# Kernel optimization log

Measured on AMD Instinct MI355X. Metric: run time of the kernel, lower is better.

## Reference

```python
import jax, jax.numpy as jnp
import numpy as np

DIM_IN, DIM_H, DIM_OUT = 1024, 512, 256
E, T, B = 8, 4, 16384


def setup_inputs() -> dict:
    key = jax.random.key(0)
    ks = jax.random.split(key, 8)
    s1 = 1.0 / np.sqrt(DIM_IN)
    s2 = 1.0 / np.sqrt(DIM_H)
    x = jax.random.normal(ks[0], (B, DIM_IN), dtype=jnp.float32)
    # stacked expert params: layer1 [E, H, IN], layer2 [E, OUT, H]
    W1 = jax.random.uniform(ks[1], (E, DIM_H, DIM_IN), jnp.float32, -s1, s1)
    b1 = jax.random.uniform(ks[2], (E, DIM_H), jnp.float32, -s1, s1)
    W2 = jax.random.uniform(ks[3], (E, DIM_OUT, DIM_H), jnp.float32, -s2, s2)
    b2 = jax.random.uniform(ks[4], (E, DIM_OUT), jnp.float32, -s2, s2)
    # gate params: [T, E, IN]
    Wg = jax.random.uniform(ks[5], (T, E, DIM_IN), jnp.float32, -s1, s1)
    bg = jax.random.uniform(ks[6], (T, E), jnp.float32, -s1, s1)
    return {"x": x, "W1": W1, "b1": b1, "W2": W2, "b2": b2, "Wg": Wg, "bg": bg}


def reference(x, W1, b1, W2, b2, Wg, bg):
    # Experts: Linear+ReLU, Linear+ReLU (dropout=0 / eval mode)
    h = jax.nn.relu(jnp.einsum('bi,ehi->beh', x, W1) + b1)          # [B,E,H]
    feats = jax.nn.relu(jnp.einsum('beh,edh->bed', h, W2) + b2)     # [B,E,D]
    # Gates: softmax over experts, one gate per task
    logits = jnp.einsum('bi,tei->bte', x, Wg) + bg                  # [B,T,E]
    w = jax.nn.softmax(logits, axis=-1)                             # [B,T,E]
    # Weighted combine: einsum('bde,be->bd') per task
    out = jnp.einsum('bed,bte->tbd', feats, w)                      # [T,B,D]
    return out
```

## Files before the change

### kernel.cpp

```cpp
#include <hip/hip_runtime.h>


typedef __attribute__((ext_vector_type(8))) __bf16 bf16x8;
typedef __attribute__((ext_vector_type(4))) float f32x4;
typedef __attribute__((ext_vector_type(8))) unsigned short u16x8;

__device__ __forceinline__ float bf2f(unsigned short u) {
  union { unsigned int i; float f; } x;
  x.i = ((unsigned int)u) << 16;
  return x.f;
}

__device__ __forceinline__ unsigned short f2bf(float f) {
  union { float f; unsigned int i; } x;
  x.f = f;
  unsigned int r = x.i + 0x7FFFu + ((x.i >> 16) & 1u);
  return (unsigned short)(r >> 16);
}

__device__ __forceinline__ void gload_lds16(const unsigned short* g, unsigned short* l) {
  __builtin_amdgcn_global_load_lds(
      (const __attribute__((address_space(1))) void*)g,
      (__attribute__((address_space(3))) void*)l, 16, 0, 0);
}

__global__ void cvt_k(const float* __restrict__ in, unsigned short* __restrict__ out, int n4) {
  int i = blockIdx.x * blockDim.x + threadIdx.x;
  if (i >= n4) return;
  float4 v = ((const float4*)in)[i];
  ushort4 o;
  o.x = f2bf(v.x); o.y = f2bf(v.y); o.z = f2bf(v.z); o.w = f2bf(v.w);
  ((ushort4*)out)[i] = o;
}

__global__ __launch_bounds__(256) void gates_k(
    const unsigned short* __restrict__ xb,
    const unsigned short* __restrict__ Wgb,
    const float* __restrict__ bg,
    float* __restrict__ gw)
{
  const int lane = threadIdx.x & 63;
  const int wid = threadIdx.x >> 6;
  const int wgid = blockIdx.x * 4 + wid;
  const int brow = wgid * 16;
  const int l15 = lane & 15, lhi = lane >> 4;

  f32x4 acc0 = {0.f, 0.f, 0.f, 0.f};
  f32x4 acc1 = {0.f, 0.f, 0.f, 0.f};
  for (int k0 = 0; k0 < 1024; k0 += 32) {
    bf16x8 a  = *(const bf16x8*)&xb[(size_t)(brow + l15) * 1024 + k0 + lhi * 8];
    bf16x8 b0 = *(const bf16x8*)&Wgb[(size_t)l15 * 1024 + k0 + lhi * 8];
    bf16x8 b1 = *(const bf16x8*)&Wgb[(size_t)(16 + l15) * 1024 + k0 + lhi * 8];
    acc0 = __builtin_amdgcn_mfma_f32_16x16x32_bf16(a, b0, acc0, 0, 0, 0);
    acc1 = __builtin_amdgcn_mfma_f32_16x16x32_bf16(a, b1, acc1, 0, 0, 0);
  }
  const float bg0 = bg[l15];
  const float bg1 = bg[16 + l15];
#pragma unroll
  for (int r = 0; r < 4; ++r) {
    float v0 = acc0[r] + bg0;
    float v1 = acc1[r] + bg1;
    float m0 = v0, m1 = v1;
#pragma unroll
    for (int d = 1; d <= 4; d <<= 1) {
      m0 = fmaxf(m0, __shfl_xor(m0, d));
      m1 = fmaxf(m1, __shfl_xor(m1, d));
    }
    float e0 = __expf(v0 - m0), e1 = __expf(v1 - m1);
    float s0 = e0, s1 = e1;
#pragma unroll
    for (int d = 1; d <= 4; d <<= 1) {
      s0 += __shfl_xor(s0, d);
      s1 += __shfl_xor(s1, d);
    }
    int b = brow + lhi * 4 + r;
    gw[(size_t)b * 32 + l15]      = e0 / s0;
    gw[(size_t)b * 32 + 16 + l15] = e1 / s1;
  }
}

template <bool RELU>
__global__ __launch_bounds__(512, 2) void gemm256(
    const unsigned short* __restrict__ A, int lda, int aZ,
    const unsigned short* __restrict__ B,
    const float* __restrict__ bias,
    unsigned short* __restrict__ C, int ldc, int cZ,
    int tilesN, int N, int K)
{
  extern __shared__ char smem_raw[];
  unsigned short* lds = (unsigned short*)smem_raw;
  char* ldsb = (char*)smem_raw;

  const int tid = threadIdx.x;
  const int lane = tid & 63, wid = tid >> 6;
  const int wr = wid >> 2, wc = wid & 3;
  const int l15 = lane & 15, lhi = lane >> 4;

  const int nwg = gridDim.x;
  const int cpx = nwg >> 3;
  const int wg = blockIdx.x;
  const int swz = (wg & 7) * cpx + (wg >> 3);
  const int rt = swz / tilesN, ct = swz - rt * tilesN;
  const int brow = rt * 256, bcol = ct * 256;
  const int e = blockIdx.z;

  const unsigned short* Ab = A + (size_t)e * aZ + (size_t)brow * lda;
  const unsigned short* Bb = B + (size_t)e * N * K + (size_t)bcol * K;
  const float* biasb = bias + (size_t)e * N;
  unsigned short* Cb = C + (size_t)e * cZ;

  const int NT = K >> 6;
  const int NI = NT >> 1;

  const int trow = tid >> 3;
  const int cg8 = (((tid & 7) ^ (trow & 7)) << 3);

  const int axor = (l15 & 7) << 4;
  const int koff0 = (lhi << 4) ^ axor;
  const int koff1 = (64 + (lhi << 4)) ^ axor;

  const char* pA0 = ldsb + wr * 16384 + l15 * 128 + koff0;
  const char* pA1 = ldsb + wr * 16384 + l15 * 128 + koff1;
  const char* pB0 = ldsb + 65536 + wc * 8192 + l15 * 128 + koff0;
  const char* pB1 = ldsb + 65536 + wc * 8192 + l15 * 128 + koff1;

  const f32x4 zero = {0.f, 0.f, 0.f, 0.f};
  f32x4 acc[8][4];
#pragma unroll
  for (int m = 0; m < 8; ++m)
#pragma unroll
    for (int n = 0; n < 4; ++n) acc[m][n] = zero;

  auto STAGE_A = [&](int slot, int t, int u) {
    gload_lds16(Ab + (size_t)(u * 64 + trow) * lda + (t * 64 + cg8),
                lds + slot * 16384 + u * 4096 + wid * 512);
  };
  auto STAGE_B = [&](int slot, int t, int u) {
    gload_lds16(Bb + (size_t)(u * 64 + trow) * K + (t * 64 + cg8),
                lds + 32768 + slot * 16384 + u * 4096 + wid * 512);
  };

#pragma unroll
  for (int u = 0; u < 4; ++u) STAGE_B(0, 0, u);
  STAGE_A(0, 0, 0); STAGE_A(0, 0, 2);
  STAGE_A(0, 0, 1); STAGE_A(0, 0, 3);
#pragma unroll
  for (int u = 0; u < 4; ++u) STAGE_B(1, 1, u);
  asm volatile("s_waitcnt vmcnt(6)" ::: "memory");
  __builtin_amdgcn_s_barrier();

  auto ktile = [&](int slot, int t) {
    const bool stA = (t + 1) < NT;
    const bool stB = (t + 2) < NT;
    bf16x8 af[4][2], bfr[4][2];

#pragma unroll
    for (int mi = 0; mi < 4; ++mi) {
      af[mi][0] = *(const bf16x8*)(pA0 + slot * 32768 + mi * 2048);
      af[mi][1] = *(const bf16x8*)(pA1 + slot * 32768 + mi * 2048);
    }
#pragma unroll
    for (int n = 0; n < 2; ++n) {
      bfr[n][0] = *(const bf16x8*)(pB0 + slot * 32768 + n * 2048);
      bfr[n][1] = *(const bf16x8*)(pB1 + slot * 32768 + n * 2048);
    }
    if (stA) { STAGE_A(slot ^ 1, t + 1, 0); STAGE_A(slot ^ 1, t + 1, 2); }
    __builtin_amdgcn_s_barrier();
    __builtin_amdgcn_s_setprio(1);
#pragma unroll
    for (int kk = 0; kk < 2; ++kk)
#pragma unroll
      for (int mi = 0; mi < 4; ++mi)
#pragma unroll
        for (int n = 0; n < 2; ++n)
          acc[mi][n] = __builtin_amdgcn_mfma_f32_16x16x32_bf16(bfr[n][kk], af[mi][kk], acc[mi][n], 0, 0, 0);
    __builtin_amdgcn_s_setprio(0);
    __builtin_amdgcn_s_barrier();

#pragma unroll
    for (int n = 0; n < 2; ++n) {
      bfr[2 + n][0] = *(const bf16x8*)(pB0 + slot * 32768 + (2 + n) * 2048);
      bfr[2 + n][1] = *(const bf16x8*)(pB1 + slot * 32768 + (2 + n) * 2048);
    }
    if (stA) { STAGE_A(slot ^ 1, t + 1, 1); STAGE_A(slot ^ 1, t + 1, 3); }
    __builtin_amdgcn_s_barrier();
    __builtin_amdgcn_s_setprio(1);
#pragma unroll
    for (int kk = 0; kk < 2; ++kk)
#pragma unroll
      for (int mi = 0; mi < 4; ++mi)
#pragma unroll
        for (int n = 0; n < 2; ++n)
          acc[mi][2 + n] = __builtin_amdgcn_mfma_f32_16x16x32_bf16(bfr[2 + n][kk], af[mi][kk], acc[mi][2 + n], 0, 0, 0);
    __builtin_amdgcn_s_setprio(0);
    if (stA) asm volatile("s_waitcnt vmcnt(8)" ::: "memory");
    else     asm volatile("s_waitcnt vmcnt(0)" ::: "memory");
    __builtin_amdgcn_s_barrier();

#pragma unroll
    for (int mi = 0; mi < 4; ++mi) {
      af[mi][0] = *(const bf16x8*)(pA0 + slot * 32768 + 8192 + mi * 2048);
      af[mi][1] = *(const bf16x8*)(pA1 + slot * 32768 + 8192 + mi * 2048);
    }
    if (stB) { STAGE_B(slot, t + 2, 0); STAGE_B(slot, t + 2, 1); }
    __builtin_amdgcn_s_barrier();
    __builtin_amdgcn_s_setprio(1);
#pragma unroll
    for (int kk = 0; kk < 2; ++kk)
#pragma unroll
      for (int mi = 0; mi < 4; ++mi)
#pragma unroll
        for (int n = 0; n < 2; ++n)
          acc[4 + mi][n] = __builtin_amdgcn_mfma_f32_16x16x32_bf16(bfr[n][kk], af[mi][kk], acc[4 + mi][n], 0, 0, 0);
    __builtin_amdgcn_s_setprio(0);
    __builtin_amdgcn_s_barrier();

    if (stB) { STAGE_B(slot, t + 2, 2); STAGE_B(slot, t + 2, 3); }
    __builtin_amdgcn_s_barrier();
    __builtin_amdgcn_s_setprio(1);
#pragma unroll
    for (int kk = 0; kk < 2; ++kk)
#pragma unroll
      for (int mi = 0; mi < 4; ++mi)
#pragma unroll
        for (int n = 0; n < 2; ++n)
          acc[4 + mi][2 + n] = __builtin_amdgcn_mfma_f32_16x16x32_bf16(bfr[2 + n][kk], af[mi][kk], acc[4 + mi][2 + n], 0, 0, 0);
    __builtin_amdgcn_s_setprio(0);
    if (stB) {
      asm volatile("s_waitcnt vmcnt(6)" ::: "memory");
      __builtin_amdgcn_s_barrier();
    } else if (stA) {
      asm volatile("s_waitcnt vmcnt(2)" ::: "memory");
      __builtin_amdgcn_s_barrier();
    }
  };

#pragma unroll 1
  for (int i = 0; i < NI; ++i) {
    ktile(0, 2 * i);
    ktile(1, 2 * i + 1);
  }

  f32x4 bias4[4];
#pragma unroll
  for (int nf = 0; nf < 4; ++nf)
    bias4[nf] = *(const f32x4*)&biasb[bcol + wc * 64 + nf * 16 + lhi * 4];

#pragma unroll
  for (int mf = 0; mf < 8; ++mf) {
    const size_t rowoff = (size_t)(brow + wr * 128 + mf * 16 + l15) * ldc;
#pragma unroll
    for (int nf = 0; nf < 4; ++nf) {
      const int col = bcol + wc * 64 + nf * 16 + lhi * 4;
      f32x4 v = acc[mf][nf];
      ushort4 o;
      float v0 = v[0] + bias4[nf][0];
      float v1 = v[1] + bias4[nf][1];
      float v2 = v[2] + bias4[nf][2];
      float v3 = v[3] + bias4[nf][3];
      if (RELU) {
        v0 = v0 > 0.f ? v0 : 0.f;
        v1 = v1 > 0.f ? v1 : 0.f;
        v2 = v2 > 0.f ? v2 : 0.f;
        v3 = v3 > 0.f ? v3 : 0.f;
      }
      o.x = f2bf(v0); o.y = f2bf(v1); o.z = f2bf(v2); o.w = f2bf(v3);
      *(ushort4*)&Cb[rowoff + col] = o;
    }
  }
}

template <bool RELU>
__global__ __launch_bounds__(256) void gemm_bt(
    const unsigned short* __restrict__ A, int lda, int aZ,
    const unsigned short* __restrict__ B,
    const float* __restrict__ bias,
    unsigned short* __restrict__ C, int ldc, int cZ,
    int N, int K)
{
  __shared__ unsigned short As[128 * 64];
  __shared__ unsigned short Bs[128 * 64];
  const int tid = threadIdx.x;
  const int wid = tid >> 6;
  const int lane = tid & 63;
  const int wr = wid >> 1, wc = wid & 1;
  const int l15 = lane & 15, lhi = lane >> 4;
  const int brow = blockIdx.x * 128;
  const int bcol = blockIdx.y * 128;
  const int e = blockIdx.z;

  const unsigned short* Ab = A + (size_t)e * aZ;
  const unsigned short* Bb = B + (size_t)e * N * K;
  const float* biasb = bias + (size_t)e * N;
  unsigned short* Cb = C + (size_t)e * cZ;

  const f32x4 zero = {0.f, 0.f, 0.f, 0.f};
  f32x4 acc[4][4];
#pragma unroll
  for (int m = 0; m < 4; ++m)
#pragma unroll
    for (int n = 0; n < 4; ++n) acc[m][n] = zero;

  const int srow = lane >> 3;
  const int scol = (lane & 7) * 8;
  const int rbase = wid * 32;

  for (int k0 = 0; k0 < K; k0 += 64) {
#pragma unroll
    for (int i = 0; i < 4; ++i) {
      int r = rbase + i * 8;
      gload_lds16(Ab + (size_t)(brow + r + srow) * lda + (k0 + scol), &As[r * 64]);
    }
#pragma unroll
    for (int i = 0; i < 4; ++i) {
      int r = rbase + i * 8;
      gload_lds16(Bb + (size_t)(bcol + r + srow) * K + (k0 + scol), &Bs[r * 64]);
    }
    __syncthreads();
#pragma unroll
    for (int kk = 0; kk < 2; ++kk) {
      bf16x8 af[4], bfr[4];
#pragma unroll
      for (int m = 0; m < 4; ++m)
        af[m] = *(const bf16x8*)&As[(wr * 64 + m * 16 + l15) * 64 + kk * 32 + lhi * 8];
#pragma unroll
      for (int n = 0; n < 4; ++n)
        bfr[n] = *(const bf16x8*)&Bs[(wc * 64 + n * 16 + l15) * 64 + kk * 32 + lhi * 8];
#pragma unroll
      for (int m = 0; m < 4; ++m)
#pragma unroll
        for (int n = 0; n < 4; ++n)
          acc[m][n] = __builtin_amdgcn_mfma_f32_16x16x32_bf16(af[m], bfr[n], acc[m][n], 0, 0, 0);
    }
    __syncthreads();
  }

#pragma unroll
  for (int n = 0; n < 4; ++n) {
    int col = bcol + wc * 64 + n * 16 + l15;
    float bv = biasb[col];
#pragma unroll
    for (int m = 0; m < 4; ++m) {
      int row0 = brow + wr * 64 + m * 16 + lhi * 4;
#pragma unroll
      for (int r = 0; r < 4; ++r) {
        float v = acc[m][n][r] + bv;
        if (RELU) v = v > 0.f ? v : 0.f;
        Cb[(size_t)(row0 + r) * ldc + col] = f2bf(v);
      }
    }
  }
}

__global__ __launch_bounds__(256) void combine_k(
    const unsigned short* __restrict__ feats,
    const float* __restrict__ gw,
    float* __restrict__ out)
{
  int tid = blockIdx.x * 256 + threadIdx.x;
  int b = tid >> 5;
  int d0 = (tid & 31) * 8;

  const f32x4* wv4 = (const f32x4*)(gw + (size_t)b * 32);
  f32x4 wv[8];
#pragma unroll
  for (int i = 0; i < 8; ++i) wv[i] = wv4[i];

  float o[4][8];
#pragma unroll
  for (int t = 0; t < 4; ++t)
#pragma unroll
    for (int j = 0; j < 8; ++j) o[t][j] = 0.f;

#pragma unroll
  for (int e = 0; e < 8; ++e) {
    u16x8 fv = *(const u16x8*)&feats[((size_t)b * 8 + e) * 256 + d0];
    float f[8];
#pragma unroll
    for (int j = 0; j < 8; ++j) f[j] = bf2f(fv[j]);
#pragma unroll
    for (int t = 0; t < 4; ++t) {
      float wt = wv[(t * 8 + e) >> 2][(t * 8 + e) & 3];
#pragma unroll
      for (int j = 0; j < 8; ++j) o[t][j] += wt * f[j];
    }
  }
#pragma unroll
  for (int t = 0; t < 4; ++t) {
    f32x4* dst = (f32x4*)(out + ((size_t)t * 16384 + b) * 256 + d0);
    f32x4 s0 = {o[t][0], o[t][1], o[t][2], o[t][3]};
    f32x4 s1 = {o[t][4], o[t][5], o[t][6], o[t][7]};
    dst[0] = s0;
    dst[1] = s1;
  }
}

extern "C" void kernel_launch(void* const* d_in, const int* in_sizes, int n_in,
                              void* d_out, int out_size, void* d_ws, size_t ws_size,
                              hipStream_t stream) {
  (void)in_sizes; (void)n_in; (void)out_size; (void)ws_size;
  const float* x  = (const float*)d_in[0];
  const float* W1 = (const float*)d_in[1];
  const float* b1 = (const float*)d_in[2];
  const float* W2 = (const float*)d_in[3];
  const float* b2 = (const float*)d_in[4];
  const float* Wg = (const float*)d_in[5];
  const float* bg = (const float*)d_in[6];
  float* out = (float*)d_out;

  char* ws = (char*)d_ws;
  unsigned short* xb    = (unsigned short*)ws; ws += (size_t)16384 * 1024 * 2;
  unsigned short* W1b   = (unsigned short*)ws; ws += (size_t)4096 * 1024 * 2;
  unsigned short* W2b   = (unsigned short*)ws; ws += (size_t)2048 * 512 * 2;
  unsigned short* Wgb   = (unsigned short*)ws; ws += (size_t)32 * 1024 * 2;
  float*          gw    = (float*)ws;         ws += (size_t)16384 * 32 * 4;
  unsigned short* H     = (unsigned short*)ws; ws += (size_t)16384 * 4096 * 2;
  unsigned short* feats = (unsigned short*)ws; ws += (size_t)16384 * 2048 * 2;

  cvt_k<<<16384, 256, 0, stream>>>(x, xb, 16384 * 1024 / 4);
  cvt_k<<<4096, 256, 0, stream>>>(W1, W1b, 4096 * 1024 / 4);
  cvt_k<<<1024, 256, 0, stream>>>(W2, W2b, 2048 * 512 / 4);
  cvt_k<<<32, 256, 0, stream>>>(Wg, Wgb, 32 * 1024 / 4);

  gates_k<<<256, 256, 0, stream>>>(xb, Wgb, bg, gw);

  gemm256<true><<<dim3(1024, 1, 1), 512, 131072, stream>>>(
      xb, 1024, 0, W1b, b1, H, 4096, 0, 16, 4096, 1024);

  gemm_bt<true><<<dim3(128, 2, 8), 256, 0, stream>>>(
      H, 4096, 512, W2b, b2, feats, 2048, 256, 256, 512);

  combine_k<<<2048, 256, 0, stream>>>(feats, gw, out);
}
```

Measured before the change: 285.6 us.

## Restructure gemm256 prefetch to stage full next tile, remap gemm_bt block order

The large first-layer GEMM's software pipeline changes from staggered A/B prefetch (A one tile ahead, B two ahead) to a simpler scheme. The full A and B of the next k-tile are staged into the alternate slot during the current tile, and the waitcnt values are fixed. The bias loads move ahead of the main loop. The second GEMM's launch becomes a 1D grid per expert with a swizzled block-to-tile mapping, so that blocks sharing rows of H run close together, for better L2 reuse. The shallower prefetch may expose more memory latency in the first GEMM.

```diff
diff --git a/kernel.cpp b/kernel.cpp
--- a/kernel.cpp
+++ b/kernel.cpp
@@ -124,6 +124,11 @@
   const char* pB0 = ldsb + 65536 + wc * 8192 + l15 * 128 + koff0;
   const char* pB1 = ldsb + 65536 + wc * 8192 + l15 * 128 + koff1;
 
+  f32x4 bias4[4];
+#pragma unroll
+  for (int nf = 0; nf < 4; ++nf)
+    bias4[nf] = *(const f32x4*)&biasb[bcol + wc * 64 + nf * 16 + lhi * 4];
+
   const f32x4 zero = {0.f, 0.f, 0.f, 0.f};
   f32x4 acc[8][4];
 #pragma unroll
@@ -142,18 +147,13 @@
 
 #pragma unroll
   for (int u = 0; u < 4; ++u) STAGE_B(0, 0, u);
-  STAGE_A(0, 0, 0); STAGE_A(0, 0, 2);
-  STAGE_A(0, 0, 1); STAGE_A(0, 0, 3);
-#pragma unroll
-  for (int u = 0; u < 4; ++u) STAGE_B(1, 1, u);
-  asm volatile("s_waitcnt vmcnt(6)" ::: "memory");
+#pragma unroll
+  for (int u = 0; u < 4; ++u) STAGE_A(0, 0, u);
+  asm volatile("s_waitcnt vmcnt(0)" ::: "memory");
   __builtin_amdgcn_s_barrier();
 
-  auto ktile = [&](int slot, int t) {
-    const bool stA = (t + 1) < NT;
-    const bool stB = (t + 2) < NT;
+  auto ktile = [&](int slot, int tn, bool stageNext) {
     bf16x8 af[4][2], bfr[4][2];
-
 #pragma unroll
     for (int mi = 0; mi < 4; ++mi) {
       af[mi][0] = *(const bf16x8*)(pA0 + slot * 32768 + mi * 2048);
@@ -164,7 +164,7 @@
       bfr[n][0] = *(const bf16x8*)(pB0 + slot * 32768 + n * 2048);
       bfr[n][1] = *(const bf16x8*)(pB1 + slot * 32768 + n * 2048);
     }
-    if (stA) { STAGE_A(slot ^ 1, t + 1, 0); STAGE_A(slot ^ 1, t + 1, 2); }
+    if (stageNext) { STAGE_B(slot ^ 1, tn, 0); STAGE_B(slot ^ 1, tn, 1); }
     __builtin_amdgcn_s_barrier();
     __builtin_amdgcn_s_setprio(1);
 #pragma unroll
@@ -182,7 +182,7 @@
       bfr[2 + n][0] = *(const bf16x8*)(pB0 + slot * 32768 + (2 + n) * 2048);
       bfr[2 + n][1] = *(const bf16x8*)(pB1 + slot * 32768 + (2 + n) * 2048);
     }
-    if (stA) { STAGE_A(slot ^ 1, t + 1, 1); STAGE_A(slot ^ 1, t + 1, 3); }
+    if (stageNext) { STAGE_B(slot ^ 1, tn, 2); STAGE_B(slot ^ 1, tn, 3); }
     __builtin_amdgcn_s_barrier();
     __builtin_amdgcn_s_setprio(1);
 #pragma unroll
@@ -193,8 +193,7 @@
         for (int n = 0; n < 2; ++n)
           acc[mi][2 + n] = __builtin_amdgcn_mfma_f32_16x16x32_bf16(bfr[2 + n][kk], af[mi][kk], acc[mi][2 + n], 0, 0, 0);
     __builtin_amdgcn_s_setprio(0);
-    if (stA) asm volatile("s_waitcnt vmcnt(8)" ::: "memory");
-    else     asm volatile("s_waitcnt vmcnt(0)" ::: "memory");
+    asm volatile("s_waitcnt vmcnt(4)" ::: "memory");
     __builtin_amdgcn_s_barrier();
 
 #pragma unroll
@@ -202,7 +201,7 @@
       af[mi][0] = *(const bf16x8*)(pA0 + slot * 32768 + 8192 + mi * 2048);
       af[mi][1] = *(const bf16x8*)(pA1 + slot * 32768 + 8192 + mi * 2048);
     }
-    if (stB) { STAGE_B(slot, t + 2, 0); STAGE_B(slot, t + 2, 1); }
+    if (stageNext) { STAGE_A(slot ^ 1, tn, 0); STAGE_A(slot ^ 1, tn, 2); }
     __builtin_amdgcn_s_barrier();
     __builtin_amdgcn_s_setprio(1);
 #pragma unroll
@@ -215,7 +214,7 @@
     __builtin_amdgcn_s_setprio(0);
     __builtin_amdgcn_s_barrier();
 
-    if (stB) { STAGE_B(slot, t + 2, 2); STAGE_B(slot, t + 2, 3); }
+    if (stageNext) { STAGE_A(slot ^ 1, tn, 1); STAGE_A(slot ^ 1, tn, 3); }
     __builtin_amdgcn_s_barrier();
     __builtin_amdgcn_s_setprio(1);
 #pragma unroll
@@ -226,25 +225,15 @@
         for (int n = 0; n < 2; ++n)
           acc[4 + mi][2 + n] = __builtin_amdgcn_mfma_f32_16x16x32_bf16(bfr[2 + n][kk], af[mi][kk], acc[4 + mi][2 + n], 0, 0, 0);
     __builtin_amdgcn_s_setprio(0);
-    if (stB) {
-      asm volatile("s_waitcnt vmcnt(6)" ::: "memory");
-      __builtin_amdgcn_s_barrier();
-    } else if (stA) {
-      asm volatile("s_waitcnt vmcnt(2)" ::: "memory");
-      __builtin_amdgcn_s_barrier();
-    }
+    asm volatile("s_waitcnt vmcnt(2)" ::: "memory");
+    __builtin_amdgcn_s_barrier();
   };
 
 #pragma unroll 1
   for (int i = 0; i < NI; ++i) {
-    ktile(0, 2 * i);
-    ktile(1, 2 * i + 1);
-  }
-
-  f32x4 bias4[4];
-#pragma unroll
-  for (int nf = 0; nf < 4; ++nf)
-    bias4[nf] = *(const f32x4*)&biasb[bcol + wc * 64 + nf * 16 + lhi * 4];
+    ktile(0, 2 * i + 1, true);
+    ktile(1, 2 * i + 2, (2 * i + 2) < NT);
+  }
 
 #pragma unroll
   for (int mf = 0; mf < 8; ++mf) {
@@ -285,8 +274,9 @@
   const int lane = tid & 63;
   const int wr = wid >> 1, wc = wid & 1;
   const int l15 = lane & 15, lhi = lane >> 4;
-  const int brow = blockIdx.x * 128;
-  const int bcol = blockIdx.y * 128;
+  const int b = blockIdx.x;
+  const int brow = (((b >> 4) << 3) + (b & 7)) * 128;
+  const int bcol = ((b >> 3) & 1) * 128;
   const int e = blockIdx.z;
 
   const unsigned short* Ab = A + (size_t)e * aZ;
@@ -427,7 +417,7 @@
   gemm256<true><<<dim3(1024, 1, 1), 512, 131072, stream>>>(
       xb, 1024, 0, W1b, b1, H, 4096, 0, 16, 4096, 1024);
 
-  gemm_bt<true><<<dim3(128, 2, 8), 256, 0, stream>>>(
+  gemm_bt<true><<<dim3(256, 1, 8), 256, 0, stream>>>(
       H, 4096, 512, W2b, b2, feats, 2048, 256, 256, 512);
 
   combine_k<<<2048, 256, 0, stream>>>(feats, gw, out);
```

Result: no change. 287.2 us (+0.6%).
